# Kernel optimization log

Hardware: AMD Instinct MI355X
Metric: run time of the kernel (lower is better)

Reference implementation:

```python
import jax, jax.numpy as jnp
import numpy as np

B = 32768
H = 512
NH = 8
EPS = 1e-5


def _glorot(key, shape):
    fan_in, fan_out = shape[-1], shape[0]
    lim = (6.0 / (fan_in + fan_out)) ** 0.5
    return jax.random.uniform(key, shape, jnp.float32, -lim, lim)


def setup_inputs() -> dict:
    key = jax.random.key(0)
    ks = jax.random.split(key, 32)
    d = {
        "graph_features": jax.random.normal(ks[0], (B, H), jnp.float32),
        "seq_features": jax.random.normal(ks[1], (B, H), jnp.float32),
        "tabular_features": jax.random.normal(ks[2], (B, H), jnp.float32),
    }
    i = 3
    for name in ("g2s", "s2g", "t2m"):
        d[f"{name}_w_in"] = _glorot(ks[i], (3 * H, H)); i += 1
        d[f"{name}_b_in"] = jnp.zeros((3 * H,), jnp.float32)
        d[f"{name}_w_out"] = _glorot(ks[i], (H, H)); i += 1
        d[f"{name}_b_out"] = jnp.zeros((H,), jnp.float32)
    for name in ("gate_g", "gate_s", "gate_t"):
        d[f"{name}_w"] = _glorot(ks[i], (H, 2 * H)); i += 1
        d[f"{name}_b"] = jnp.zeros((H,), jnp.float32)
    d["fc1_w"] = _glorot(ks[i], (2 * H, 3 * H)); i += 1
    d["fc1_b"] = jnp.zeros((2 * H,), jnp.float32)
    d["ln_g"] = jnp.ones((2 * H,), jnp.float32)
    d["ln_b"] = jnp.zeros((2 * H,), jnp.float32)
    d["fc2_w"] = _glorot(ks[i], (H, 2 * H)); i += 1
    d["fc2_b"] = jnp.zeros((H,), jnp.float32)
    return d


def _mha(q, k, v, w_in, b_in, w_out, b_out):
    # q: [B,Sq,H], k/v: [B,Sk,H]. PyTorch nn.MultiheadAttention math (eval mode).
    dh = H // NH
    qp = q @ w_in[:H].T + b_in[:H]
    kp = k @ w_in[H:2 * H].T + b_in[H:2 * H]
    vp = v @ w_in[2 * H:].T + b_in[2 * H:]
    qh = qp.reshape(qp.shape[0], qp.shape[1], NH, dh)
    kh = kp.reshape(kp.shape[0], kp.shape[1], NH, dh)
    vh = vp.reshape(vp.shape[0], vp.shape[1], NH, dh)
    scores = jnp.einsum("bqhd,bkhd->bhqk", qh, kh) / jnp.sqrt(jnp.float32(dh))
    attn = jax.nn.softmax(scores, axis=-1)
    out = jnp.einsum("bhqk,bkhd->bqhd", attn, vh).reshape(q.shape[0], q.shape[1], H)
    return out @ w_out.T + b_out


def reference(graph_features, seq_features, tabular_features,
              g2s_w_in, g2s_b_in, g2s_w_out, g2s_b_out,
              s2g_w_in, s2g_b_in, s2g_w_out, s2g_b_out,
              t2m_w_in, t2m_b_in, t2m_w_out, t2m_b_out,
              gate_g_w, gate_g_b, gate_s_w, gate_s_b, gate_t_w, gate_t_b,
              fc1_w, fc1_b, ln_g, ln_b, fc2_w, fc2_b):
    g = graph_features[:, None, :]   # [B,1,H]
    s = seq_features[:, None, :]
    t = tabular_features[:, None, :]

    graph_to_seq = _mha(s, g, g, g2s_w_in, g2s_b_in, g2s_w_out, g2s_b_out)
    seq_to_graph = _mha(g, s, s, s2g_w_in, s2g_b_in, s2g_w_out, s2g_b_out)

    graph_gate = jax.nn.sigmoid(jnp.concatenate([g, seq_to_graph], -1) @ gate_g_w.T + gate_g_b)
    seq_gate = jax.nn.sigmoid(jnp.concatenate([s, graph_to_seq], -1) @ gate_s_w.T + gate_s_b)
    gated_graph = g * graph_gate
    gated_seq = s * seq_gate

    multimodal = jnp.concatenate([gated_graph, gated_seq], axis=1)  # [B,2,H]
    t2m = _mha(multimodal, t, t, t2m_w_in, t2m_b_in, t2m_w_out, t2m_b_out)  # [B,2,H]

    tab_comb = jnp.concatenate([t, t2m.mean(axis=1, keepdims=True)], -1)
    tab_gate = jax.nn.sigmoid(tab_comb @ gate_t_w.T + gate_t_b)
    gated_tab = t * tab_gate

    allf = jnp.concatenate([gated_graph[:, 0], gated_seq[:, 0], gated_tab[:, 0]], -1)  # [B,3H]
    h = allf @ fc1_w.T + fc1_b
    mu = h.mean(-1, keepdims=True)
    var = ((h - mu) ** 2).mean(-1, keepdims=True)
    h = (h - mu) / jnp.sqrt(var + EPS) * ln_g + ln_b
    h = jax.nn.relu(h)
    return h @ fc2_w.T + fc2_b
```

## Files before the change

### kernel.cpp

```cpp
#include <hip/hip_runtime.h>
#include <stdint.h>
#include <stddef.h>

#define MROWS 32768
#define HDIM  512
#define CH    16384
#define BM 128
#define BN 128
#define BK 64

typedef __attribute__((ext_vector_type(8))) _Float16 half8;
typedef __attribute__((ext_vector_type(4))) _Float16 half4v;
typedef __attribute__((ext_vector_type(4))) float    f32x4;

static __device__ __forceinline__ void gld_lds16(const void* g, void* l) {
    __builtin_amdgcn_global_load_lds(
        (__attribute__((address_space(1))) void*)(uintptr_t)g,
        (__attribute__((address_space(3))) void*)(uint32_t)(uintptr_t)l,
        16, 0, 0);
}

struct CvtJob  { const float* src; _Float16* dst; int srcld4, dstld, rowlen4, rows; };
struct CvtJobs { CvtJob j[11]; };

__global__ __launch_bounds__(256)
void cvt_rows(CvtJobs J) {
    const CvtJob jb = J.j[blockIdx.y];
    const int row = blockIdx.x;
    if (row >= jb.rows) return;
    const float4* __restrict__ s = (const float4*)jb.src + (size_t)row * jb.srcld4;
    _Float16* __restrict__ d = jb.dst + (size_t)row * jb.dstld;
    for (int c = threadIdx.x; c < jb.rowlen4; c += 256) {
        const float4 v = s[c];
        half4v o = { (_Float16)v.x, (_Float16)v.y, (_Float16)v.z, (_Float16)v.w };
        *(half4v*)(d + c * 4) = o;
    }
}

__global__ __launch_bounds__(384)
void cvt_chunk3(const float* __restrict__ x0, const float* __restrict__ x1,
                const float* __restrict__ x2, _Float16* __restrict__ dst) {
    const int row = blockIdx.x;
    const int mod = threadIdx.x >> 7;
    const int c   = threadIdx.x & 127;
    const float* s = (mod == 0) ? x0 : (mod == 1) ? x1 : x2;
    const float4 v = ((const float4*)(s + (size_t)row * 512))[c];
    half4v o = { (_Float16)v.x, (_Float16)v.y, (_Float16)v.z, (_Float16)v.w };
    *(half4v*)(dst + (size_t)row * 1536 + mod * 512 + c * 4) = o;
}

struct TcvtArgs { const float* src[3]; _Float16* dst; };
__global__ __launch_bounds__(256)
void tcvt512(TcvtArgs a) {
    __shared__ float t[32][33];
    const int m = blockIdx.z;
    const float* __restrict__ src = a.src[m];
    _Float16* __restrict__ dst = a.dst + (size_t)m * HDIM * HDIM;
    const int bx = blockIdx.x * 32, by = blockIdx.y * 32;
    const int tx = threadIdx.x & 31, ty = threadIdx.x >> 5;
    #pragma unroll
    for (int q = 0; q < 4; ++q)
        t[ty + q * 8][tx] = src[(size_t)(by + ty + q * 8) * 512 + bx + tx];
    __syncthreads();
    #pragma unroll
    for (int q = 0; q < 4; ++q)
        dst[(size_t)(bx + ty + q * 8) * 512 + by + tx] = (_Float16)t[tx][ty + q * 8];
}

struct MvArgs { const float* W[3]; const float* x[3]; const float* b[3]; float* y; int ldw, woff; };
__global__ __launch_bounds__(256)
void mv3(MvArgs a) {
    const int m = blockIdx.y;
    const int i = blockIdx.x * 256 + threadIdx.x;
    const float* __restrict__ W = a.W[m] + (size_t)i * a.ldw + a.woff;
    const float* __restrict__ x = a.x[m];
    float s = a.b[m][i];
    for (int j = 0; j < 512; ++j) s += W[j] * x[j];
    a.y[m * 512 + i] = s;
}

struct GemmP {
    const void* A1;
    const _Float16* W; const float* bias; void* C;
    int K, ldA1, ldw, ldc, coff;
    int zsA, zsW, zsC;
};

template<int EPI, int OCC>
__global__ __launch_bounds__(256, OCC)
void gemm_k(GemmP p) {
    __shared__ __align__(16) unsigned char smem[32768];
    _Float16* Asm = (_Float16*)smem;
    _Float16* Bsm = (_Float16*)(smem + 16384);

    const int tid  = threadIdx.x;
    const int wid  = tid >> 6;
    const int lane = tid & 63;
    const int m0 = blockIdx.x * BM;
    const int n0 = blockIdx.y * BN;
    const ptrdiff_t zz = (ptrdiff_t)blockIdx.z;
    const _Float16* __restrict__ A1h = (const _Float16*)((const char*)p.A1 + zz * p.zsA);
    const _Float16* __restrict__ Wp  = (const _Float16*)((const char*)p.W + zz * p.zsW);
    char* Cz = (char*)p.C + zz * p.zsC;

    const int wr = (wid >> 1) * 64;
    const int wc = (wid & 1) * 64;
    const int l15 = lane & 15;
    const int lhi = lane >> 4;

    f32x4 acc[4][4] = {};

    for (int kt = 0; kt < p.K; kt += BK) {
        #pragma unroll
        for (int i = 0; i < 4; ++i) {
            const int seg = wid * 256 + i * 64 + lane;
            const int row = seg >> 3;
            const int ke  = (seg & 7) * 8;
            gld_lds16(Wp  + (size_t)(n0 + row) * p.ldw  + kt + ke, &Bsm[seg * 8]);
            gld_lds16(A1h + (size_t)(m0 + row) * p.ldA1 + kt + ke, &Asm[seg * 8]);
        }
        __syncthreads();
        #pragma unroll
        for (int kk = 0; kk < BK; kk += 32) {
            half8 fa[4], fb[4];
            #pragma unroll
            for (int i = 0; i < 4; ++i) {
                fa[i] = *(const half8*)&Asm[(wr + i * 16 + l15) * BK + kk + lhi * 8];
                fb[i] = *(const half8*)&Bsm[(wc + i * 16 + l15) * BK + kk + lhi * 8];
            }
            #pragma unroll
            for (int i = 0; i < 4; ++i)
                #pragma unroll
                for (int j = 0; j < 4; ++j)
                    acc[i][j] = __builtin_amdgcn_mfma_f32_16x16x32_f16(fa[i], fb[j], acc[i][j], 0, 0, 0);
        }
        __syncthreads();
    }

    if (EPI == 3) {
        float* Cf = (float*)smem;
        float* __restrict__ C = (float*)Cz;
        #pragma unroll
        for (int h = 0; h < 2; ++h) {
            if ((wr >> 6) == h) {
                #pragma unroll
                for (int j = 0; j < 4; ++j) {
                    const int col = wc + j * 16 + l15;
                    const float bia = p.bias ? p.bias[n0 + col] : 0.f;
                    #pragma unroll
                    for (int i = 0; i < 4; ++i)
                        #pragma unroll
                        for (int r = 0; r < 4; ++r)
                            Cf[(i * 16 + lhi * 4 + r) * 128 + col] = acc[i][j][r] + bia;
                }
            }
            __syncthreads();
            #pragma unroll
            for (int pph = 0; pph < 8; ++pph) {
                const int seg = pph * 256 + tid;
                const int row = seg >> 5, cs = seg & 31;
                const float4 v = *(const float4*)&Cf[row * 128 + cs * 4];
                *(float4*)&C[(size_t)(m0 + h * 64 + row) * p.ldc + n0 + cs * 4] = v;
            }
            __syncthreads();
        }
    } else {
        _Float16* Ct = (_Float16*)smem;
        #pragma unroll
        for (int j = 0; j < 4; ++j) {
            const int col = wc + j * 16 + l15;
            const float bia = (EPI == 2) ? 0.f : (p.bias ? p.bias[n0 + col] : 0.f);
            #pragma unroll
            for (int i = 0; i < 4; ++i)
                #pragma unroll
                for (int r = 0; r < 4; ++r) {
                    float v = acc[i][j][r] + bia;
                    if (EPI == 1) v = 1.f / (1.f + __expf(-v));
                    Ct[(wr + i * 16 + lhi * 4 + r) * 128 + col] = (_Float16)v;
                }
        }
        __syncthreads();
        _Float16* __restrict__ C = (_Float16*)Cz;
        #pragma unroll
        for (int pph = 0; pph < 8; ++pph) {
            const int seg = pph * 256 + tid;
            const int row = seg >> 4, cs = seg & 15;
            half8 hv = *(const half8*)&Ct[row * 128 + cs * 8];
            const size_t cidx = (size_t)(m0 + row) * p.ldc + p.coff + n0 + cs * 8;
            if (EPI == 1) {
                const half8 xv = *(const half8*)(A1h + (size_t)(m0 + row) * p.ldA1
                                                 + n0 + cs * 8);
                hv = hv * xv;
            }
            if (EPI == 2) { const half8 old = *(const half8*)&C[cidx]; hv = hv + old; }
            *(half8*)&C[cidx] = hv;
        }
    }
}

struct Gemm8P {
    const _Float16* A; const _Float16* W; const float* bias; _Float16* C;
    int K, ldA, ldW, ldc, coff;
};

template<int EPI>
__global__ __launch_bounds__(512, 1)
void gemm8(Gemm8P p) {
    __shared__ __align__(16) unsigned char lds[131072];
    char* LA = (char*)lds;
    char* LB = (char*)lds + 65536;

    const int tid  = threadIdx.x;
    const int wid  = tid >> 6;
    const int lane = tid & 63;
    const int wm = wid >> 2;
    const int wn = wid & 3;
    const int l15 = lane & 15;
    const int lhi = lane >> 4;
    const int m0 = blockIdx.x * 256;
    const int n0 = blockIdx.y * 256;
    const _Float16* __restrict__ A = p.A;
    const _Float16* __restrict__ W = p.W;
    const int ldA = p.ldA, ldW = p.ldW;
    const int nT = p.K >> 6;

    f32x4 acc[8][4] = {};

    auto stageh = [&](const _Float16* src, int ld, int r0, char* base, int t, int kh) {
        const int q = t & 1;
        const int kt = t * 64 + kh * 32;
        char* dst = base + (size_t)(q * 2 + kh) * 16384;
        #pragma unroll
        for (int k = 0; k < 2; ++k) {
            const int j = tid + k * 512;
            const int row = j >> 2, i = j & 3;
            const int kc = i ^ ((row >> 1) & 3);
            gld_lds16(src + (size_t)(r0 + row) * ld + kt + kc * 8,
                      dst + (size_t)j * 16);
        }
    };
    #define STAGE8(t, kh) { stageh(A, ldA, m0, LA, (t), (kh)); stageh(W, ldW, n0, LB, (t), (kh)); }

    STAGE8(0, 0);
    STAGE8(0, 1);
    if (nT > 1) { STAGE8(1, 0); asm volatile("s_waitcnt vmcnt(8)" ::: "memory"); }
    else        {               asm volatile("s_waitcnt vmcnt(0)" ::: "memory"); }
    __builtin_amdgcn_s_barrier();
    asm volatile("" ::: "memory");

    for (int t = 0; t < nT; ++t) {
        const int q = t & 1;
        half8 fb[4];
        #pragma unroll
        for (int ph = 0; ph < 4; ++ph) {
            const int kh = ph >> 1, g = ph & 1;
            const char* ra = LA + (size_t)(q * 2 + kh) * 16384;
            const char* rb = LB + (size_t)(q * 2 + kh) * 16384;
            half8 fa[4];
            if (g == 0) {
                #pragma unroll
                for (int nf = 0; nf < 4; ++nf) {
                    const int row = wn * 64 + nf * 16 + l15;
                    const int sl = lhi ^ ((row >> 1) & 3);
                    fb[nf] = *(const half8*)(rb + ((size_t)row * 4 + sl) * 16);
                }
            }
            #pragma unroll
            for (int mi = 0; mi < 4; ++mi) {
                const int row = wm * 128 + (g * 4 + mi) * 16 + l15;
                const int sl = lhi ^ ((row >> 1) & 3);
                fa[mi] = *(const half8*)(ra + ((size_t)row * 4 + sl) * 16);
            }
            if (ph == 0 && t + 1 < nT) STAGE8(t + 1, 1);
            if (ph == 2 && t + 2 < nT) STAGE8(t + 2, 0);
            asm volatile("s_waitcnt lgkmcnt(0)" ::: "memory");
            __builtin_amdgcn_sched_barrier(0);
            __builtin_amdgcn_s_setprio(1);
            #pragma unroll
            for (int mi = 0; mi < 4; ++mi)
                #pragma unroll
                for (int nf = 0; nf < 4; ++nf)
                    acc[g * 4 + mi][nf] = __builtin_amdgcn_mfma_f32_16x16x32_f16(
                        fa[mi], fb[nf], acc[g * 4 + mi][nf], 0, 0, 0);
            __builtin_amdgcn_s_setprio(0);
            if (ph == 1) {
                if (t + 1 < nT) asm volatile("s_waitcnt vmcnt(8)" ::: "memory");
                else            asm volatile("s_waitcnt vmcnt(0)" ::: "memory");
            }
            if (ph == 3) {
                if (t + 2 < nT)      asm volatile("s_waitcnt vmcnt(8)" ::: "memory");
                else if (t + 1 < nT) asm volatile("s_waitcnt vmcnt(4)" ::: "memory");
            }
            asm volatile("" ::: "memory");
            __builtin_amdgcn_s_barrier();
            asm volatile("" ::: "memory");
        }
    }

    _Float16* Ct = (_Float16*)lds;
    #pragma unroll
    for (int mf = 0; mf < 8; ++mf)
        #pragma unroll
        for (int nf = 0; nf < 4; ++nf) {
            const int col = wn * 64 + nf * 16 + l15;
            const float bia = p.bias[n0 + col];
            #pragma unroll
            for (int r = 0; r < 4; ++r) {
                float v = acc[mf][nf][r] + bia;
                if (EPI == 1) v = 1.f / (1.f + __expf(-v));
                Ct[(wm * 128 + mf * 16 + lhi * 4 + r) * 256 + col] = (_Float16)v;
            }
        }
    __syncthreads();
    #pragma unroll
    for (int it = 0; it < 16; ++it) {
        const int u = it * 512 + tid;
        const int row = u >> 5, cs = u & 31;
        half8 hv = *(const half8*)&Ct[row * 256 + cs * 8];
        if (EPI == 1) {
            const half8 xv = *(const half8*)(A + (size_t)(m0 + row) * ldA + n0 + cs * 8);
            hv = hv * xv;
        }
        *(half8*)&p.C[(size_t)(m0 + row) * p.ldc + p.coff + n0 + cs * 8] = hv;
    }
}

__global__ __launch_bounds__(256)
void ln_relu(const _Float16* __restrict__ hin, _Float16* __restrict__ hout,
             const float* __restrict__ gamma, const float* __restrict__ beta) {
    const int row  = blockIdx.x * 4 + (threadIdx.x >> 6);
    const int lane = threadIdx.x & 63;
    const _Float16* hr = hin + (size_t)row * 1024;
    _Float16* ho = hout + (size_t)row * 1024;
    const half8 v0 = *(const half8*)(hr + lane * 8);
    const half8 v1 = *(const half8*)(hr + 512 + lane * 8);
    float f0[8], f1[8];
    float s = 0.f, s2 = 0.f;
    #pragma unroll
    for (int j = 0; j < 8; ++j) {
        f0[j] = (float)v0[j]; s += f0[j]; s2 += f0[j] * f0[j];
        f1[j] = (float)v1[j]; s += f1[j]; s2 += f1[j] * f1[j];
    }
    #pragma unroll
    for (int off = 32; off > 0; off >>= 1) {
        s  += __shfl_xor(s,  off, 64);
        s2 += __shfl_xor(s2, off, 64);
    }
    const float mean = s * (1.f / 1024.f);
    const float var  = s2 * (1.f / 1024.f) - mean * mean;
    const float rstd = rsqrtf(var + 1e-5f);
    half8 o0, o1;
    #pragma unroll
    for (int j = 0; j < 8; ++j) {
        const int i0 = lane * 8 + j, i1 = 512 + lane * 8 + j;
        const float av = (f0[j] - mean) * rstd * gamma[i0] + beta[i0];
        const float bv = (f1[j] - mean) * rstd * gamma[i1] + beta[i1];
        o0[j] = (_Float16)(av > 0.f ? av : 0.f);
        o1[j] = (_Float16)(bv > 0.f ? bv : 0.f);
    }
    *(half8*)(ho + lane * 8) = o0;
    *(half8*)(ho + 512 + lane * 8) = o1;
}

extern "C" void kernel_launch(void* const* d_in, const int* in_sizes, int n_in,
                              void* d_out, int out_size, void* d_ws, size_t ws_size,
                              hipStream_t stream)
{
    (void)in_sizes; (void)n_in; (void)out_size;
    const size_t HH = (size_t)HDIM * HDIM;

    _Float16* wsH   = (_Float16*)d_ws;
    _Float16* slotB = wsH;
    _Float16* Xch   = slotB + (size_t)CH * 1536;
    _Float16* Wouth = Xch   + (size_t)CH * 1536;
    _Float16* Wg2h  = Wouth + 3 * HH;
    _Float16* WvT   = Wg2h  + 3 * HH;
    _Float16* WcoT  = WvT   + 3 * HH;
    _Float16* Wbig  = WcoT  + 3 * HH;
    _Float16* Wc2   = Wbig  + 4 * HH;
    _Float16* fc1h  = Wc2   + 1 * HH;
    _Float16* fc2h  = fc1h  + 6 * HH;
    float*    bco   = (float*)(fc2h + 2 * HH);
    float*    beff  = bco + 3 * 512;
    _Float16* hws   = wsH;
    const size_t need = (size_t)((char*)(beff + 3 * 512) - (char*)d_ws);
    if (ws_size < need) return;

    const float* X[3] = { (const float*)d_in[0], (const float*)d_in[1], (const float*)d_in[2] };
    const int asrc[3] = { 1, 0, 2 };

    CvtJobs cj;
    for (int m = 0; m < 3; ++m) {
        cj.j[m]     = { (const float*)d_in[5 + 4 * m], Wouth + m * HH, 128, 512, 128, 512 };
        cj.j[3 + m] = { (const float*)d_in[15 + 2 * m] + 512, Wg2h + m * HH, 256, 512, 128, 512 };
    }
    cj.j[6]  = { (const float*)d_in[15], Wbig,                    256, 1024, 128, 512 };
    cj.j[7]  = { (const float*)d_in[17], Wbig + 512 * 1024 + 512, 256, 1024, 128, 512 };
    cj.j[8]  = { (const float*)d_in[19], Wc2,                     256, 512,  128, 512 };
    cj.j[9]  = { (const float*)d_in[21], fc1h, 384, 1536, 384, 1024 };
    cj.j[10] = { (const float*)d_in[25], fc2h, 256, 1024, 256, 512 };
    cvt_rows<<<dim3(1024, 11, 1), 256, 0, stream>>>(cj);

    TcvtArgs ta;
    for (int m = 0; m < 3; ++m) ta.src[m] = (const float*)d_in[3 + 4 * m] + 2 * HH;
    ta.dst = WvT;
    tcvt512<<<dim3(16, 16, 3), 256, 0, stream>>>(ta);

    MvArgs mv;
    for (int m = 0; m < 3; ++m) {
        mv.W[m] = (const float*)d_in[5 + 4 * m];
        mv.x[m] = (const float*)d_in[4 + 4 * m] + 2 * HDIM;
        mv.b[m] = (const float*)d_in[6 + 4 * m];
    }
    mv.y = bco; mv.ldw = 512; mv.woff = 0;
    mv3<<<dim3(2, 3, 1), 256, 0, stream>>>(mv);

    GemmP p;
    p.bias = nullptr; p.coff = 0;
    p.zsA = p.zsW = p.zsC = 0;

    p.A1 = WvT; p.ldA1 = 512;
    p.W = Wouth; p.ldw = 512;
    p.C = WcoT; p.ldc = 512;
    p.K = 512;
    p.zsA = (int)(HH * 2); p.zsW = (int)(HH * 2); p.zsC = (int)(HH * 2);
    gemm_k<0, 4><<<dim3(4, 4, 3), 256, 0, stream>>>(p);

    p.A1 = Wg2h; p.zsA = (int)(HH * 2);
    p.W = WcoT + HH; p.zsW = -(int)(HH * 2);
    p.C = Wbig + 512; p.ldc = 1024; p.zsC = (int)((512 * 1024 - 512) * 2);
    gemm_k<0, 4><<<dim3(4, 4, 2), 256, 0, stream>>>(p);

    p.A1 = Wg2h + 2 * HH; p.zsA = 0;
    p.W = WcoT + 2 * HH; p.zsW = 0;
    p.C = Wc2; p.ldc = 512; p.zsC = 0;
    gemm_k<2, 4><<<dim3(4, 4, 1), 256, 0, stream>>>(p);

    for (int m = 0; m < 3; ++m) {
        mv.W[m] = (const float*)d_in[15 + 2 * m];
        mv.x[m] = bco + asrc[m] * 512;
        mv.b[m] = (const float*)d_in[16 + 2 * m];
    }
    mv.y = beff; mv.ldw = 1024; mv.woff = 512;
    mv3<<<dim3(2, 3, 1), 256, 0, stream>>>(mv);

    _Float16* hbuf = (_Float16*)d_out;
    Gemm8P g8;
    for (int c = 0; c < 2; ++c) {
        const size_t roff = (size_t)c * CH;

        cvt_chunk3<<<dim3(CH, 1, 1), 384, 0, stream>>>(
            X[0] + roff * HDIM, X[1] + roff * HDIM, X[2] + roff * HDIM, Xch);

        g8.A = Xch; g8.ldA = 1536;
        g8.W = Wbig; g8.ldW = 1024;
        g8.bias = beff;
        g8.C = slotB; g8.ldc = 1536; g8.coff = 0;
        g8.K = 1024;
        gemm8<1><<<dim3(CH / 256, 4, 1), 512, 0, stream>>>(g8);

        p.A1 = Xch + 1024; p.ldA1 = 1536;
        p.W = Wc2; p.ldw = 512;
        p.bias = beff + 1024;
        p.C = slotB; p.ldc = 1536; p.coff = 1024;
        p.K = 512; p.zsA = p.zsW = p.zsC = 0;
        gemm_k<1, 4><<<dim3(CH / BM, 4, 1), 256, 0, stream>>>(p);

        g8.A = slotB; g8.ldA = 1536;
        g8.W = fc1h; g8.ldW = 1536;
        g8.bias = (const float*)d_in[22];
        g8.C = hbuf + roff * 1024; g8.ldc = 1024; g8.coff = 0;
        g8.K = 1536;
        gemm8<0><<<dim3(CH / 256, 4, 1), 512, 0, stream>>>(g8);
    }

    ln_relu<<<dim3(MROWS / 4, 1, 1), 256, 0, stream>>>(
        hbuf, hws, (const float*)d_in[23], (const float*)d_in[24]);

    p.A1 = hws; p.ldA1 = 1024;
    p.W = fc2h; p.ldw = 1024;
    p.bias = (const float*)d_in[26];
    p.C = d_out; p.ldc = HDIM; p.coff = 0;
    p.K = 1024; p.zsA = p.zsW = p.zsC = 0;
    gemm_k<3, 4><<<dim3(MROWS / BM, HDIM / BN, 1), 256, 0, stream>>>(p);
}
```

Baseline: 466.2 us.

## Run fc2 on the 256x256 gemm8 kernel and load full K-half fragments at once

The final fc2 GEMM moves from the 128x128 gemm_k kernel to the 256x256, 512-thread gemm8 kernel. A new fp32-output epilogue (EPI 3) stages results through LDS in two 128-row halves. The gemm8 inner loop is also restructured from four phases to two K-halves, each loading all 8 A fragments and 4 B fragments before 32 MFMAs. This cuts barriers and waitcnts per tile at the cost of higher register pressure. The larger tile aims to improve operand reuse for fc2, but with MROWS/256 x 2 the grid is only 256 blocks, which may underfill the GPU.

```diff
diff --git a/kernel.cpp b/kernel.cpp
--- a/kernel.cpp
+++ b/kernel.cpp
@@ -199,7 +199,7 @@
 }
 
 struct Gemm8P {
-    const _Float16* A; const _Float16* W; const float* bias; _Float16* C;
+    const _Float16* A; const _Float16* W; const float* bias; void* C;
     int K, ldA, ldW, ldc, coff;
 };
 
@@ -250,44 +250,39 @@
 
     for (int t = 0; t < nT; ++t) {
         const int q = t & 1;
-        half8 fb[4];
-        #pragma unroll
-        for (int ph = 0; ph < 4; ++ph) {
-            const int kh = ph >> 1, g = ph & 1;
+        #pragma unroll
+        for (int kh = 0; kh < 2; ++kh) {
             const char* ra = LA + (size_t)(q * 2 + kh) * 16384;
             const char* rb = LB + (size_t)(q * 2 + kh) * 16384;
-            half8 fa[4];
-            if (g == 0) {
-                #pragma unroll
-                for (int nf = 0; nf < 4; ++nf) {
-                    const int row = wn * 64 + nf * 16 + l15;
-                    const int sl = lhi ^ ((row >> 1) & 3);
-                    fb[nf] = *(const half8*)(rb + ((size_t)row * 4 + sl) * 16);
-                }
-            }
-            #pragma unroll
-            for (int mi = 0; mi < 4; ++mi) {
-                const int row = wm * 128 + (g * 4 + mi) * 16 + l15;
+            half8 fa[8], fb[4];
+            #pragma unroll
+            for (int nf = 0; nf < 4; ++nf) {
+                const int row = wn * 64 + nf * 16 + l15;
                 const int sl = lhi ^ ((row >> 1) & 3);
-                fa[mi] = *(const half8*)(ra + ((size_t)row * 4 + sl) * 16);
-            }
-            if (ph == 0 && t + 1 < nT) STAGE8(t + 1, 1);
-            if (ph == 2 && t + 2 < nT) STAGE8(t + 2, 0);
+                fb[nf] = *(const half8*)(rb + ((size_t)row * 4 + sl) * 16);
+            }
+            #pragma unroll
+            for (int mf = 0; mf < 8; ++mf) {
+                const int row = wm * 128 + mf * 16 + l15;
+                const int sl = lhi ^ ((row >> 1) & 3);
+                fa[mf] = *(const half8*)(ra + ((size_t)row * 4 + sl) * 16);
+            }
+            if (kh == 0 && t + 1 < nT) STAGE8(t + 1, 1);
+            if (kh == 1 && t + 2 < nT) STAGE8(t + 2, 0);
             asm volatile("s_waitcnt lgkmcnt(0)" ::: "memory");
             __builtin_amdgcn_sched_barrier(0);
             __builtin_amdgcn_s_setprio(1);
             #pragma unroll
-            for (int mi = 0; mi < 4; ++mi)
+            for (int mf = 0; mf < 8; ++mf)
                 #pragma unroll
                 for (int nf = 0; nf < 4; ++nf)
-                    acc[g * 4 + mi][nf] = __builtin_amdgcn_mfma_f32_16x16x32_f16(
-                        fa[mi], fb[nf], acc[g * 4 + mi][nf], 0, 0, 0);
+                    acc[mf][nf] = __builtin_amdgcn_mfma_f32_16x16x32_f16(
+                        fa[mf], fb[nf], acc[mf][nf], 0, 0, 0);
             __builtin_amdgcn_s_setprio(0);
-            if (ph == 1) {
+            if (kh == 0) {
                 if (t + 1 < nT) asm volatile("s_waitcnt vmcnt(8)" ::: "memory");
                 else            asm volatile("s_waitcnt vmcnt(0)" ::: "memory");
-            }
-            if (ph == 3) {
+            } else {
                 if (t + 2 < nT)      asm volatile("s_waitcnt vmcnt(8)" ::: "memory");
                 else if (t + 1 < nT) asm volatile("s_waitcnt vmcnt(4)" ::: "memory");
             }
@@ -297,31 +292,61 @@
         }
     }
 
-    _Float16* Ct = (_Float16*)lds;
-    #pragma unroll
-    for (int mf = 0; mf < 8; ++mf)
-        #pragma unroll
-        for (int nf = 0; nf < 4; ++nf) {
-            const int col = wn * 64 + nf * 16 + l15;
-            const float bia = p.bias[n0 + col];
-            #pragma unroll
-            for (int r = 0; r < 4; ++r) {
-                float v = acc[mf][nf][r] + bia;
-                if (EPI == 1) v = 1.f / (1.f + __expf(-v));
-                Ct[(wm * 128 + mf * 16 + lhi * 4 + r) * 256 + col] = (_Float16)v;
-            }
-        }
-    __syncthreads();
-    #pragma unroll
-    for (int it = 0; it < 16; ++it) {
-        const int u = it * 512 + tid;
-        const int row = u >> 5, cs = u & 31;
-        half8 hv = *(const half8*)&Ct[row * 256 + cs * 8];
-        if (EPI == 1) {
-            const half8 xv = *(const half8*)(A + (size_t)(m0 + row) * ldA + n0 + cs * 8);
-            hv = hv * xv;
-        }
-        *(half8*)&p.C[(size_t)(m0 + row) * p.ldc + p.coff + n0 + cs * 8] = hv;
+    if (EPI == 3) {
+        float* Cf = (float*)lds;
+        float* __restrict__ C = (float*)p.C;
+        #pragma unroll
+        for (int h = 0; h < 2; ++h) {
+            if (wm == h) {
+                #pragma unroll
+                for (int mf = 0; mf < 8; ++mf)
+                    #pragma unroll
+                    for (int nf = 0; nf < 4; ++nf) {
+                        const int col = wn * 64 + nf * 16 + l15;
+                        const float bia = p.bias[n0 + col];
+                        #pragma unroll
+                        for (int r = 0; r < 4; ++r)
+                            Cf[(mf * 16 + lhi * 4 + r) * 256 + col] = acc[mf][nf][r] + bia;
+                    }
+            }
+            __syncthreads();
+            #pragma unroll
+            for (int it = 0; it < 16; ++it) {
+                const int u = it * 512 + tid;
+                const int row = u >> 6, cs = u & 63;
+                const float4 v = *(const float4*)&Cf[row * 256 + cs * 4];
+                *(float4*)&C[(size_t)(m0 + h * 128 + row) * p.ldc + n0 + cs * 4] = v;
+            }
+            __syncthreads();
+        }
+    } else {
+        _Float16* Ct = (_Float16*)lds;
+        _Float16* __restrict__ C = (_Float16*)p.C;
+        #pragma unroll
+        for (int mf = 0; mf < 8; ++mf)
+            #pragma unroll
+            for (int nf = 0; nf < 4; ++nf) {
+                const int col = wn * 64 + nf * 16 + l15;
+                const float bia = p.bias[n0 + col];
+                #pragma unroll
+                for (int r = 0; r < 4; ++r) {
+                    float v = acc[mf][nf][r] + bia;
+                    if (EPI == 1) v = 1.f / (1.f + __expf(-v));
+                    Ct[(wm * 128 + mf * 16 + lhi * 4 + r) * 256 + col] = (_Float16)v;
+                }
+            }
+        __syncthreads();
+        #pragma unroll
+        for (int it = 0; it < 16; ++it) {
+            const int u = it * 512 + tid;
+            const int row = u >> 5, cs = u & 31;
+            half8 hv = *(const half8*)&Ct[row * 256 + cs * 8];
+            if (EPI == 1) {
+                const half8 xv = *(const half8*)(A + (size_t)(m0 + row) * ldA + n0 + cs * 8);
+                hv = hv * xv;
+            }
+            *(half8*)&C[(size_t)(m0 + row) * p.ldc + p.coff + n0 + cs * 8] = hv;
+        }
     }
 }
 
@@ -477,10 +502,10 @@
     ln_relu<<<dim3(MROWS / 4, 1, 1), 256, 0, stream>>>(
         hbuf, hws, (const float*)d_in[23], (const float*)d_in[24]);
 
-    p.A1 = hws; p.ldA1 = 1024;
-    p.W = fc2h; p.ldw = 1024;
-    p.bias = (const float*)d_in[26];
-    p.C = d_out; p.ldc = HDIM; p.coff = 0;
-    p.K = 1024; p.zsA = p.zsW = p.zsC = 0;
-    gemm_k<3, 4><<<dim3(MROWS / BM, HDIM / BN, 1), 256, 0, stream>>>(p);
-}
+    g8.A = hws; g8.ldA = 1024;
+    g8.W = fc2h; g8.ldW = 1024;
+    g8.bias = (const float*)d_in[26];
+    g8.C = d_out; g8.ldc = HDIM; g8.coff = 0;
+    g8.K = 1024;
+    gemm8<3><<<dim3(MROWS / 256, HDIM / 256, 1), 512, 0, stream>>>(g8);
+}
```

Measured after the change: 454.6 us. -2.5%, faster.
